# Kernel optimization log

Hardware: AMD Instinct MI355X
Metric: run time of the kernel (lower is better)

## Reference

```python
import jax, jax.numpy as jnp
import numpy as np

EMBED_DIM = 256
NUM_HEADS = 4
LN_EPS = 1e-5


def setup_inputs() -> dict:
    b, n, e = 2, 4096, EMBED_DIM
    key = jax.random.key(0)
    ks = jax.random.split(key, 12)
    x = jax.random.normal(ks[0], (b, n, e), dtype=jnp.float32)
    # rotary cache: cos/sin of random angles, shape [2, b, n, e, 1]
    ang = jax.random.uniform(ks[1], (b, n, e, 1), dtype=jnp.float32) * (2 * np.pi)
    encoding = jnp.stack([jnp.cos(ang), jnp.sin(ang)], axis=0)
    s_e = 1.0 / np.sqrt(e)
    s_2e = 1.0 / np.sqrt(2 * e)
    Wqkv_w = jax.random.normal(ks[2], (3 * e, e), dtype=jnp.float32) * s_e
    Wqkv_b = jax.random.normal(ks[3], (3 * e,), dtype=jnp.float32) * s_e
    out_w = jax.random.normal(ks[4], (e, e), dtype=jnp.float32) * s_e
    out_b = jax.random.normal(ks[5], (e,), dtype=jnp.float32) * s_e
    ffn1_w = jax.random.normal(ks[6], (2 * e, 2 * e), dtype=jnp.float32) * s_2e
    ffn1_b = jax.random.normal(ks[7], (2 * e,), dtype=jnp.float32) * s_2e
    ln_g = jnp.ones((2 * e,), dtype=jnp.float32)
    ln_b = jnp.zeros((2 * e,), dtype=jnp.float32)
    ffn2_w = jax.random.normal(ks[8], (e, 2 * e), dtype=jnp.float32) * s_2e
    ffn2_b = jax.random.normal(ks[9], (e,), dtype=jnp.float32) * s_2e
    return {"x": x, "encoding": encoding, "Wqkv_w": Wqkv_w, "Wqkv_b": Wqkv_b,
            "out_w": out_w, "out_b": out_b, "ffn1_w": ffn1_w, "ffn1_b": ffn1_b,
            "ln_g": ln_g, "ln_b": ln_b, "ffn2_w": ffn2_w, "ffn2_b": ffn2_b}


def _forward(x, encoding, Wqkv_w, Wqkv_b, out_w, out_b, ffn1_w, ffn1_b, ln_g, ln_b, ffn2_w, ffn2_b):
    b, n, e = x.shape
    h = NUM_HEADS
    hd = e // h
    qkv = x @ Wqkv_w.T + Wqkv_b                      # [b,n,3e]
    qkv = qkv.reshape(b, n, e, 3)
    qk, v = qkv[..., :2], qkv[..., 2]                # [b,n,e,2], [b,n,e]
    # rotate_half: interpret e as (h, hd//2, 2) pairs, rotate within pairs
    r = qk.reshape(b, n, h, hd // 2, 2, 2)
    r = jnp.stack([-r[..., 1, :], r[..., 0, :]], axis=4).reshape(b, n, e, 2)
    qk = qk * encoding[0] + r * encoding[1]          # cached rotary emb
    q = qk[..., 0].reshape(b, n, h, hd)
    k = qk[..., 1].reshape(b, n, h, hd)
    vh = v.reshape(b, n, h, hd)
    scale = 1.0 / np.sqrt(hd).astype(np.float32)
    scores = jnp.einsum('bqhd,bkhd->bhqk', q, k) * scale
    attn = jax.nn.softmax(scores, axis=-1)
    ctx = jnp.einsum('bhqk,bkhd->bqhd', attn, vh).reshape(b, n, e)
    message = ctx @ out_w.T + out_b
    y = jnp.concatenate([x, message], axis=2)        # [b,n,2e]
    y = y @ ffn1_w.T + ffn1_b
    mu = jnp.mean(y, axis=-1, keepdims=True)
    var = jnp.mean(jnp.square(y - mu), axis=-1, keepdims=True)
    y = (y - mu) * jax.lax.rsqrt(var + LN_EPS) * ln_g + ln_b
    y = jax.nn.gelu(y, approximate=False)            # torch nn.GELU default = exact
    y = y @ ffn2_w.T + ffn2_b
    return x + y


def reference(x, encoding, Wqkv_w, Wqkv_b, out_w, out_b, ffn1_w, ffn1_b, ln_g, ln_b, ffn2_w, ffn2_b):
    return _forward(x, encoding, Wqkv_w, Wqkv_b, out_w, out_b, ffn1_w, ffn1_b, ln_g, ln_b, ffn2_w, ffn2_b)
```

## Files before the change

### kernel.cpp

```cpp
#include <hip/hip_runtime.h>
#include <hip/hip_bf16.h>

using u16 = unsigned short;
using u16x8 = __attribute__((ext_vector_type(8))) unsigned short;
using s16x4 = __attribute__((ext_vector_type(4))) short;
using s16x8 = __attribute__((ext_vector_type(8))) short;
using f32x4 = __attribute__((ext_vector_type(4))) float;

__device__ __forceinline__ f32x4 mfma16(s16x8 a, s16x8 b, f32x4 c) {
    return __builtin_amdgcn_mfma_f32_16x16x32_bf16(a, b, c, 0, 0, 0);
}

__device__ __forceinline__ u16 f2bf(float f) {
    union { float f; unsigned u; } v; v.f = f;
    unsigned r = v.u + 0x7FFFu + ((v.u >> 16) & 1u);
    return (u16)(r >> 16);
}

__device__ __forceinline__ unsigned cvt_pk_bf16(float lo, float hi) {
    unsigned r;
    asm("v_cvt_pk_bf16_f32 %0, %1, %2" : "=v"(r) : "v"(lo), "v"(hi));
    return r;
}

__device__ __forceinline__ float fast_exp2(float x) {
    float r;
    asm("v_exp_f32 %0, %1" : "=v"(r) : "v"(x));
    return r;
}

__device__ __forceinline__ unsigned pk2(u16 a, u16 b) {
    return (unsigned)a | ((unsigned)b << 16);
}

__device__ __forceinline__ float bf2f(u16 u) {
    union { unsigned u; float f; } v; v.u = ((unsigned)u) << 16;
    return v.f;
}

__device__ __forceinline__ void gload_lds16(const u16* g, u16* l) {
    __builtin_amdgcn_global_load_lds(
        (const __attribute__((address_space(1))) void*)g,
        (__attribute__((address_space(3))) void*)l, 16, 0, 0);
}

__global__ __launch_bounds__(256) void conv_kernel(
    const float* __restrict__ s0, const float* __restrict__ s1,
    const float* __restrict__ s2, const float* __restrict__ s3,
    const float* __restrict__ s4,
    u16* __restrict__ d0, u16* __restrict__ d1, u16* __restrict__ d2,
    u16* __restrict__ d3, u16* __restrict__ d4)
{
    int i = blockIdx.x * 256 + threadIdx.x;
    const float* s; u16* d; int off;
    if (i < 524288)      { s = s0; d = d0; off = i; }
    else if (i < 573440) { s = s1; d = d1; off = i - 524288; }
    else if (i < 589824) { s = s2; d = d2; off = i - 573440; }
    else if (i < 655360) { s = s3; d = d3; off = i - 589824; }
    else                 { s = s4; d = d4; off = i - 655360; }
    float4 f = ((const float4*)s)[off];
    ushort4 u;
    u.x = f2bf(f.x); u.y = f2bf(f.y); u.z = f2bf(f.z); u.w = f2bf(f.w);
    ((ushort4*)d)[off] = u;
}

template<int OUTMODE, bool SPLIT, bool RESID>
__global__ __launch_bounds__(256) void gemm_kernel(
    const u16* __restrict__ A0, const u16* __restrict__ A1,
    const u16* __restrict__ W, const float* __restrict__ bias,
    const float* __restrict__ resid, float* __restrict__ outf,
    u16* __restrict__ outb, int M, int N, int K)
{
    __shared__ u16 A_lds[3][128][64];
    __shared__ u16 B_lds[3][64][64];
    const int tid = threadIdx.x;
    const int l = tid & 63, w = tid >> 6;
    const int lr = l & 15, lg = l >> 4;
    const int r7 = lr & 7;
    const int m0 = blockIdx.x * 128, n0 = blockIdx.y * 64;
    const int wm = (w >> 1) * 64, wn = (w & 1) * 32;

    const int lrow = l >> 3;
    const int swz = (l & 7) ^ lrow;
    const int arow = 32 * w + lrow;
    const int brow = 16 * w + lrow;

    #define STAGE_G(s, b)                                                     \
        do {                                                                  \
            int k0_ = 64 * (s);                                               \
            const u16* As_; int lda_;                                         \
            if (SPLIT) {                                                      \
                lda_ = 256;                                                   \
                As_ = (k0_ < 256) ? (A0 + k0_) : (A1 + (k0_ - 256));          \
            } else { lda_ = K; As_ = A0 + k0_; }                              \
            _Pragma("unroll")                                                 \
            for (int i = 0; i < 4; ++i)                                       \
                gload_lds16(As_ + (size_t)(m0 + arow + 8 * i) * lda_ + swz * 8,\
                            &A_lds[b][32 * w + 8 * i][0]);                    \
            _Pragma("unroll")                                                 \
            for (int i = 0; i < 2; ++i)                                       \
                gload_lds16(W + (size_t)(n0 + brow + 8 * i) * K + k0_ + swz * 8,\
                            &B_lds[b][16 * w + 8 * i][0]);                    \
        } while (0)

    f32x4 acc[4][2];
    #pragma unroll
    for (int i = 0; i < 4; ++i)
        #pragma unroll
        for (int j = 0; j < 2; ++j)
            acc[i][j] = (f32x4){0.f, 0.f, 0.f, 0.f};

    const int NS = K >> 6;
    int cur = 0, nxt = 1;
    STAGE_G(0, 0);

    for (int s = 0; s < NS; ++s) {
        if (s + 1 < NS) {
            STAGE_G(s + 1, nxt);
            asm volatile("s_waitcnt vmcnt(6)" ::: "memory");
        } else {
            asm volatile("s_waitcnt vmcnt(0)" ::: "memory");
        }
        __builtin_amdgcn_sched_barrier(0);
        __builtin_amdgcn_s_barrier();
        __builtin_amdgcn_sched_barrier(0);

        #pragma unroll
        for (int ks = 0; ks < 2; ++ks) {
            s16x8 af[4], bfr[2];
            #pragma unroll
            for (int ms = 0; ms < 4; ++ms)
                af[ms] = *(const s16x8*)&A_lds[cur][wm + ms * 16 + lr]
                                              [((ks * 4 + lg) ^ r7) * 8];
            #pragma unroll
            for (int ns = 0; ns < 2; ++ns)
                bfr[ns] = *(const s16x8*)&B_lds[cur][wn + ns * 16 + lr]
                                               [((ks * 4 + lg) ^ r7) * 8];
            #pragma unroll
            for (int ms = 0; ms < 4; ++ms)
                #pragma unroll
                for (int ns = 0; ns < 2; ++ns)
                    acc[ms][ns] = mfma16(af[ms], bfr[ns], acc[ms][ns]);
        }
        cur = nxt;
        nxt = (nxt == 2) ? 0 : nxt + 1;
    }
    #undef STAGE_G

    #pragma unroll
    for (int ms = 0; ms < 4; ++ms) {
        #pragma unroll
        for (int ns = 0; ns < 2; ++ns) {
            int cg = n0 + wn + ns * 16 + lr;
            float bv = bias[cg];
            #pragma unroll
            for (int r = 0; r < 4; ++r) {
                int rg = m0 + wm + ms * 16 + lg * 4 + r;
                float val = acc[ms][ns][r] + bv;
                if (RESID) val += resid[(size_t)rg * N + cg];
                if (OUTMODE == 0) outf[(size_t)rg * N + cg] = val;
                else              outb[(size_t)rg * N + cg] = f2bf(val);
            }
        }
    }
}

__global__ __launch_bounds__(256) void rope_kernel(
    const u16* __restrict__ qkv, const float* __restrict__ enc,
    u16* __restrict__ Qo, u16* __restrict__ Ko, u16* __restrict__ Vo)
{
    int idx = blockIdx.x * 256 + threadIdx.x;
    int row = idx >> 7;
    int p = idx & 127;
    int c0 = p * 2;
    const u16* base = qkv + (size_t)row * 768 + p * 6;
    ushort2 a01 = *(const ushort2*)(base);
    ushort2 a23 = *(const ushort2*)(base + 2);
    ushort2 a45 = *(const ushort2*)(base + 4);
    float q0 = bf2f(a01.x), k0 = bf2f(a01.y);
    float q1 = bf2f(a23.y), k1 = bf2f(a45.x);
    const float* cb = enc + (size_t)row * 256 + c0;
    float2 cosv = *(const float2*)cb;
    float2 sinv = *(const float2*)(cb + 2097152);
    float qr0 = q0 * cosv.x - q1 * sinv.x;
    float qr1 = q1 * cosv.y + q0 * sinv.y;
    float kr0 = k0 * cosv.x - k1 * sinv.x;
    float kr1 = k1 * cosv.y + k0 * sinv.y;
    const float qs = 0.18033688011112042f;
    qr0 *= qs; qr1 *= qs;
    int h = c0 >> 6, d = c0 & 63;
    int b = row >> 12, n = row & 4095;
    size_t o = (((size_t)(b * 4 + h)) * 4096 + n) * 64 + d;
    *(unsigned*)(Qo + o) = cvt_pk_bf16(qr0, qr1);
    *(unsigned*)(Ko + o) = cvt_pk_bf16(kr0, kr1);
    *(unsigned*)(Vo + o) = pk2(a23.x, a45.y);
}

__global__ __launch_bounds__(256) void transpose_v(
    const u16* __restrict__ V, u16* __restrict__ Vt)
{
    __shared__ u16 t[64][72];
    int bh = blockIdx.y, n0 = blockIdx.x * 64;
    int tid = threadIdx.x;
    #pragma unroll
    for (int i = 0; i < 2; ++i) {
        int c = tid + 256 * i;
        int r = c >> 3, cg = c & 7;
        *(uint4*)&t[r][cg * 8] =
            *(const uint4*)(V + ((size_t)bh * 4096 + n0 + r) * 64 + cg * 8);
    }
    __syncthreads();
    #pragma unroll
    for (int i = 0; i < 2; ++i) {
        int c = tid + 256 * i;
        int d = c >> 3, ng = c & 7;
        unsigned w0 = pk2(t[ng*8+0][d], t[ng*8+1][d]);
        unsigned w1 = pk2(t[ng*8+2][d], t[ng*8+3][d]);
        unsigned w2 = pk2(t[ng*8+4][d], t[ng*8+5][d]);
        unsigned w3 = pk2(t[ng*8+6][d], t[ng*8+7][d]);
        uint4 o4 = make_uint4(w0, w1, w2, w3);
        *(uint4*)(Vt + ((size_t)bh * 64 + d) * 4096 + n0 + ng * 8) = o4;
    }
}

__global__ __launch_bounds__(256) void attn_kernel(
    const u16* __restrict__ Qp, const u16* __restrict__ Kp,
    const u16* __restrict__ Vtp, u16* __restrict__ Opart,
    float* __restrict__ Ssum)
{
    __shared__ u16 K_lds[3][64][64];
    __shared__ u16 V_lds[3][64][64];
    const int tid = threadIdx.x;
    const int l = tid & 63, w = tid >> 6;
    const int lr = l & 15, lg = l >> 4;
    const int bh = blockIdx.y, z = blockIdx.z;
    const int n0 = blockIdx.x * 64 + w * 16;

    const u16* Qb = Qp + ((size_t)bh * 4096 + n0) * 64;
    s16x8 qf0 = *(const s16x8*)(Qb + lr * 64 + lg * 8);
    s16x8 qf1 = *(const s16x8*)(Qb + lr * 64 + 32 + lg * 8);

    const u16* Kb = Kp + (size_t)bh * 4096 * 64 + (size_t)z * 1024 * 64;
    const u16* Vb = Vtp + (size_t)bh * 64 * 4096 + z * 1024;

    const int swz = (l & 7) ^ ((l >> 3) & 7);
    const int row0 = 16 * w + (l >> 3);
    const size_t koff0 = (size_t)row0 * 64 + swz * 8;
    const size_t koff1 = (size_t)(row0 + 8) * 64 + swz * 8;
    const size_t voff0 = (size_t)row0 * 4096 + swz * 8;
    const size_t voff1 = (size_t)(row0 + 8) * 4096 + swz * 8;

    #define STAGE(kt, b)                                                      \
        do {                                                                  \
            const u16* ks_ = Kb + (size_t)(kt) * 4096;                        \
            const u16* vs_ = Vb + (size_t)(kt) * 64;                          \
            gload_lds16(ks_ + koff0, &K_lds[b][16 * w][0]);                   \
            gload_lds16(ks_ + koff1, &K_lds[b][16 * w + 8][0]);               \
            gload_lds16(vs_ + voff0, &V_lds[b][16 * w][0]);                   \
            gload_lds16(vs_ + voff1, &V_lds[b][16 * w + 8][0]);               \
        } while (0)

    f32x4 O[4];
    #pragma unroll
    for (int dv = 0; dv < 4; ++dv) O[dv] = (f32x4){0.f, 0.f, 0.f, 0.f};
    f32x4 ssum = (f32x4){0.f, 0.f, 0.f, 0.f};
    s16x8 ones;
    #pragma unroll
    for (int j = 0; j < 8; ++j) ones[j] = (short)0x3F80;

    const int r7 = lr & 7;
    int cur = 0, nxt = 1;
    STAGE(0, 0);

    for (int kt = 0; kt < 16; ++kt) {
        if (kt + 1 < 16) {
            STAGE(kt + 1, nxt);
            asm volatile("s_waitcnt vmcnt(4)" ::: "memory");
        } else {
            asm volatile("s_waitcnt vmcnt(0)" ::: "memory");
        }
        __builtin_amdgcn_sched_barrier(0);
        __builtin_amdgcn_s_barrier();
        __builtin_amdgcn_sched_barrier(0);

        f32x4 S[4];
        #pragma unroll
        for (int v4 = 0; v4 < 4; ++v4) {
            const int krow = v4 * 16 + lr;
            s16x8 kf0 = *(const s16x8*)&K_lds[cur][krow][(lg ^ r7) * 8];
            s16x8 kf1 = *(const s16x8*)&K_lds[cur][krow][((4 + lg) ^ r7) * 8];
            f32x4 zz = (f32x4){-24.f, -24.f, -24.f, -24.f};
            zz = mfma16(kf0, qf0, zz);
            zz = mfma16(kf1, qf1, zz);
            S[v4] = zz;
        }

        float p[4][4];
        #pragma unroll
        for (int v4 = 0; v4 < 4; ++v4)
            #pragma unroll
            for (int r = 0; r < 4; ++r)
                p[v4][r] = fast_exp2(S[v4][r]);

        s16x8 pa[2];
        #pragma unroll
        for (int kb = 0; kb < 2; ++kb) {
            union { unsigned u[4]; s16x8 v; } pu;
            pu.u[0] = cvt_pk_bf16(p[2*kb][0],   p[2*kb][1]);
            pu.u[1] = cvt_pk_bf16(p[2*kb][2],   p[2*kb][3]);
            pu.u[2] = cvt_pk_bf16(p[2*kb+1][0], p[2*kb+1][1]);
            pu.u[3] = cvt_pk_bf16(p[2*kb+1][2], p[2*kb+1][3]);
            pa[kb] = pu.v;
        }

        #pragma unroll
        for (int dv = 0; dv < 4; ++dv) {
            const int vrow = 16 * dv + lr;
            #pragma unroll
            for (int kb = 0; kb < 2; ++kb) {
                const int c16a = 4 * kb + (lg >> 1);
                const u16* vpa = &V_lds[cur][vrow][((c16a      ^ r7) * 8) + 4 * (lg & 1)];
                const u16* vpb = &V_lds[cur][vrow][(((c16a + 2) ^ r7) * 8) + 4 * (lg & 1)];
                s16x4 va  = *(const s16x4*)vpa;
                s16x4 vb4 = *(const s16x4*)vpb;
                s16x8 vf = __builtin_shufflevector(va, vb4, 0,1,2,3,4,5,6,7);
                O[dv] = mfma16(pa[kb], vf, O[dv]);
            }
        }
        ssum = mfma16(pa[0], ones, ssum);
        ssum = mfma16(pa[1], ones, ssum);

        cur = nxt;
        nxt = (nxt == 2) ? 0 : nxt + 1;
    }
    #undef STAGE

    u16* Ob = Opart + ((size_t)(z * 8 + bh) * 4096 + n0) * 64;
    #pragma unroll
    for (int dv = 0; dv < 4; ++dv)
        #pragma unroll
        for (int r = 0; r < 4; ++r)
            Ob[(size_t)(4 * lg + r) * 64 + 16 * dv + lr] = f2bf(O[dv][r]);
    if (lr == 0) {
        float4 sv = make_float4(ssum[0], ssum[1], ssum[2], ssum[3]);
        *(float4*)&Ssum[(size_t)(z * 8 + bh) * 4096 + n0 + 4 * lg] = sv;
    }
}

__global__ __launch_bounds__(256) void combine_kernel(
    const u16* __restrict__ Opart, const float* __restrict__ Ssum,
    u16* __restrict__ ctx)
{
    int idx = blockIdx.x * 256 + threadIdx.x;
    int rr = idx >> 3;
    int dc = (idx & 7) * 8;
    float s = Ssum[rr] + Ssum[32768 + rr] + Ssum[65536 + rr] + Ssum[98304 + rr];
    float inv = 1.f / s;
    float acc[8];
    #pragma unroll
    for (int j = 0; j < 8; ++j) acc[j] = 0.f;
    #pragma unroll
    for (int z = 0; z < 4; ++z) {
        u16x8 ov = *(const u16x8*)(Opart + ((size_t)z * 32768 + rr) * 64 + dc);
        #pragma unroll
        for (int j = 0; j < 8; ++j) acc[j] += bf2f(ov[j]);
    }
    #pragma unroll
    for (int j = 0; j < 8; ++j) acc[j] *= inv;
    int bh = rr >> 12, n = rr & 4095;
    int b = bh >> 2, h = bh & 3;
    uint4 o4 = make_uint4(cvt_pk_bf16(acc[0], acc[1]), cvt_pk_bf16(acc[2], acc[3]),
                          cvt_pk_bf16(acc[4], acc[5]), cvt_pk_bf16(acc[6], acc[7]));
    *(uint4*)(ctx + ((size_t)(b * 4096 + n)) * 256 + h * 64 + dc) = o4;
}

__global__ __launch_bounds__(256) void ln_gelu_kernel(
    const float* __restrict__ y, const float* __restrict__ g,
    const float* __restrict__ bta, u16* __restrict__ o)
{
    int row = blockIdx.x * 4 + (threadIdx.x >> 6);
    int l = threadIdx.x & 63;
    const float* yr = y + (size_t)row * 512 + l * 8;
    float4 va = *(const float4*)yr;
    float4 vb = *(const float4*)(yr + 4);
    float v[8] = {va.x, va.y, va.z, va.w, vb.x, vb.y, vb.z, vb.w};
    float s = 0.f;
    #pragma unroll
    for (int j = 0; j < 8; ++j) s += v[j];
    #pragma unroll
    for (int off = 32; off; off >>= 1) s += __shfl_xor(s, off, 64);
    float mu = s * (1.f / 512.f);
    float q = 0.f;
    #pragma unroll
    for (int j = 0; j < 8; ++j) { float t = v[j] - mu; q += t * t; }
    #pragma unroll
    for (int off = 32; off; off >>= 1) q += __shfl_xor(q, off, 64);
    float rs = rsqrtf(q * (1.f / 512.f) + 1e-5f);
    u16 u[8];
    #pragma unroll
    for (int j = 0; j < 8; ++j) {
        float t = (v[j] - mu) * rs * g[l * 8 + j] + bta[l * 8 + j];
        t = t * 0.5f * (1.f + erff(t * 0.70710678118654752f));
        u[j] = f2bf(t);
    }
    uint4 o4 = make_uint4(pk2(u[0], u[1]), pk2(u[2], u[3]),
                          pk2(u[4], u[5]), pk2(u[6], u[7]));
    *(uint4*)(o + (size_t)row * 512 + l * 8) = o4;
}

extern "C" void kernel_launch(void* const* d_in, const int* in_sizes, int n_in,
                              void* d_out, int out_size, void* d_ws, size_t ws_size,
                              hipStream_t stream) {
    (void)in_sizes; (void)n_in; (void)out_size; (void)ws_size;
    const float* x    = (const float*)d_in[0];
    const float* enc  = (const float*)d_in[1];
    const float* wqkv = (const float*)d_in[2];
    const float* bqkv = (const float*)d_in[3];
    const float* wout = (const float*)d_in[4];
    const float* bout = (const float*)d_in[5];
    const float* w1   = (const float*)d_in[6];
    const float* b1   = (const float*)d_in[7];
    const float* lng  = (const float*)d_in[8];
    const float* lnb  = (const float*)d_in[9];
    const float* w2   = (const float*)d_in[10];
    const float* b2   = (const float*)d_in[11];
    float* out = (float*)d_out;
    char* ws = (char*)d_ws;

    u16*   xb    = (u16*)(ws + 0);
    u16*   wqkvb = (u16*)(ws + 4194304);
    u16*   woutb = (u16*)(ws + 4587520);
    u16*   w1b   = (u16*)(ws + 4718592);
    u16*   w2b   = (u16*)(ws + 5242880);
    u16*   qkvb  = (u16*)(ws + 5505024);
    u16*   OpartB= (u16*)(ws + 5505024);
    float* y1    = (float*)(ws + 5505024);
    float* Ssum  = (float*)(ws + 22282240);
    u16*   q     = (u16*)(ws + 30670848);
    u16*   k     = (u16*)(ws + 34865152);
    u16*   v     = (u16*)(ws + 39059456);
    u16*   vt    = (u16*)(ws + 43253760);
    u16*   ybf   = q;
    u16*   ctx   = (u16*)(ws + 47448064);
    u16*   msg   = (u16*)(ws + 51642368);

    conv_kernel<<<2688, 256, 0, stream>>>(x, wqkv, wout, w1, w2,
                                          xb, wqkvb, woutb, w1b, w2b);
    gemm_kernel<1, false, false><<<dim3(64, 12), 256, 0, stream>>>(
        xb, nullptr, wqkvb, bqkv, nullptr, nullptr, qkvb, 8192, 768, 256);
    rope_kernel<<<4096, 256, 0, stream>>>(qkvb, enc, q, k, v);
    transpose_v<<<dim3(64, 8), 256, 0, stream>>>(v, vt);
    attn_kernel<<<dim3(64, 8, 4), 256, 0, stream>>>(q, k, vt, OpartB, Ssum);
    combine_kernel<<<1024, 256, 0, stream>>>(OpartB, Ssum, ctx);
    gemm_kernel<1, false, false><<<dim3(64, 4), 256, 0, stream>>>(
        ctx, nullptr, woutb, bout, nullptr, nullptr, msg, 8192, 256, 256);
    gemm_kernel<0, true, false><<<dim3(64, 8), 256, 0, stream>>>(
        xb, msg, w1b, b1, nullptr, y1, nullptr, 8192, 512, 512);
    ln_gelu_kernel<<<2048, 256, 0, stream>>>(y1, lng, lnb, ybf);
    gemm_kernel<0, false, true><<<dim3(64, 4), 256, 0, stream>>>(
        ybf, nullptr, w2b, b2, x, out, nullptr, 8192, 256, 512);
}
```

Baseline: 135.3 us.

## Process two query tiles per wave in attention and permute V transpose layout

Each wave now handles 32 query rows (two 16-row tiles) so every K/V fragment loaded from LDS feeds twice as many MFMAs, and the grid is halved. The V transpose stores columns in an interleaved order so the PV step can read one 8-element vector instead of two 4-element pieces. The triple-buffered pipeline with manual vmcnt waits becomes double buffering with __syncthreads, which cuts LDS use but may expose more load latency. Register pressure rises from the doubled accumulators, and the grid drops to 1024 blocks.

```diff
diff --git a/kernel.cpp b/kernel.cpp
--- a/kernel.cpp
+++ b/kernel.cpp
@@ -214,10 +214,12 @@
     for (int i = 0; i < 2; ++i) {
         int c = tid + 256 * i;
         int d = c >> 3, ng = c & 7;
-        unsigned w0 = pk2(t[ng*8+0][d], t[ng*8+1][d]);
-        unsigned w1 = pk2(t[ng*8+2][d], t[ng*8+3][d]);
-        unsigned w2 = pk2(t[ng*8+4][d], t[ng*8+5][d]);
-        unsigned w3 = pk2(t[ng*8+6][d], t[ng*8+7][d]);
+        int kb = ng >> 2, lg4 = ng & 3;
+        int base = 32 * kb + 4 * lg4;
+        unsigned w0 = pk2(t[base +  0][d], t[base +  1][d]);
+        unsigned w1 = pk2(t[base +  2][d], t[base +  3][d]);
+        unsigned w2 = pk2(t[base + 16][d], t[base + 17][d]);
+        unsigned w3 = pk2(t[base + 18][d], t[base + 19][d]);
         uint4 o4 = make_uint4(w0, w1, w2, w3);
         *(uint4*)(Vt + ((size_t)bh * 64 + d) * 4096 + n0 + ng * 8) = o4;
     }
@@ -228,17 +230,22 @@
     const u16* __restrict__ Vtp, u16* __restrict__ Opart,
     float* __restrict__ Ssum)
 {
-    __shared__ u16 K_lds[3][64][64];
-    __shared__ u16 V_lds[3][64][64];
+    __shared__ u16 K_lds[2][64][64];
+    __shared__ u16 V_lds[2][64][64];
     const int tid = threadIdx.x;
     const int l = tid & 63, w = tid >> 6;
     const int lr = l & 15, lg = l >> 4;
+    const int r7 = lr & 7;
     const int bh = blockIdx.y, z = blockIdx.z;
-    const int n0 = blockIdx.x * 64 + w * 16;
+    const int n0 = blockIdx.x * 128 + w * 32;
 
     const u16* Qb = Qp + ((size_t)bh * 4096 + n0) * 64;
-    s16x8 qf0 = *(const s16x8*)(Qb + lr * 64 + lg * 8);
-    s16x8 qf1 = *(const s16x8*)(Qb + lr * 64 + 32 + lg * 8);
+    s16x8 qf[2][2];
+    #pragma unroll
+    for (int qt = 0; qt < 2; ++qt)
+        #pragma unroll
+        for (int dh = 0; dh < 2; ++dh)
+            qf[qt][dh] = *(const s16x8*)(Qb + (qt * 16 + lr) * 64 + dh * 32 + lg * 8);
 
     const u16* Kb = Kp + (size_t)bh * 4096 * 64 + (size_t)z * 1024 * 64;
     const u16* Vb = Vtp + (size_t)bh * 64 * 4096 + z * 1024;
@@ -260,57 +267,59 @@
             gload_lds16(vs_ + voff1, &V_lds[b][16 * w + 8][0]);               \
         } while (0)
 
-    f32x4 O[4];
-    #pragma unroll
-    for (int dv = 0; dv < 4; ++dv) O[dv] = (f32x4){0.f, 0.f, 0.f, 0.f};
-    f32x4 ssum = (f32x4){0.f, 0.f, 0.f, 0.f};
+    f32x4 O[2][4];
+    #pragma unroll
+    for (int qt = 0; qt < 2; ++qt)
+        #pragma unroll
+        for (int dv = 0; dv < 4; ++dv)
+            O[qt][dv] = (f32x4){0.f, 0.f, 0.f, 0.f};
+    f32x4 ssum[2];
+    ssum[0] = (f32x4){0.f, 0.f, 0.f, 0.f};
+    ssum[1] = (f32x4){0.f, 0.f, 0.f, 0.f};
     s16x8 ones;
     #pragma unroll
     for (int j = 0; j < 8; ++j) ones[j] = (short)0x3F80;
 
-    const int r7 = lr & 7;
-    int cur = 0, nxt = 1;
     STAGE(0, 0);
+    __syncthreads();
 
     for (int kt = 0; kt < 16; ++kt) {
-        if (kt + 1 < 16) {
-            STAGE(kt + 1, nxt);
-            asm volatile("s_waitcnt vmcnt(4)" ::: "memory");
-        } else {
-            asm volatile("s_waitcnt vmcnt(0)" ::: "memory");
-        }
-        __builtin_amdgcn_sched_barrier(0);
-        __builtin_amdgcn_s_barrier();
-        __builtin_amdgcn_sched_barrier(0);
-
-        f32x4 S[4];
+        const int cur = kt & 1;
+        if (kt + 1 < 16) STAGE(kt + 1, cur ^ 1);
+
+        f32x4 S[2][4];
         #pragma unroll
         for (int v4 = 0; v4 < 4; ++v4) {
             const int krow = v4 * 16 + lr;
             s16x8 kf0 = *(const s16x8*)&K_lds[cur][krow][(lg ^ r7) * 8];
             s16x8 kf1 = *(const s16x8*)&K_lds[cur][krow][((4 + lg) ^ r7) * 8];
-            f32x4 zz = (f32x4){-24.f, -24.f, -24.f, -24.f};
-            zz = mfma16(kf0, qf0, zz);
-            zz = mfma16(kf1, qf1, zz);
-            S[v4] = zz;
-        }
-
-        float p[4][4];
-        #pragma unroll
-        for (int v4 = 0; v4 < 4; ++v4)
-            #pragma unroll
-            for (int r = 0; r < 4; ++r)
-                p[v4][r] = fast_exp2(S[v4][r]);
-
-        s16x8 pa[2];
-        #pragma unroll
-        for (int kb = 0; kb < 2; ++kb) {
-            union { unsigned u[4]; s16x8 v; } pu;
-            pu.u[0] = cvt_pk_bf16(p[2*kb][0],   p[2*kb][1]);
-            pu.u[1] = cvt_pk_bf16(p[2*kb][2],   p[2*kb][3]);
-            pu.u[2] = cvt_pk_bf16(p[2*kb+1][0], p[2*kb+1][1]);
-            pu.u[3] = cvt_pk_bf16(p[2*kb+1][2], p[2*kb+1][3]);
-            pa[kb] = pu.v;
+            #pragma unroll
+            for (int qt = 0; qt < 2; ++qt) {
+                f32x4 zz = (f32x4){-24.f, -24.f, -24.f, -24.f};
+                zz = mfma16(kf0, qf[qt][0], zz);
+                zz = mfma16(kf1, qf[qt][1], zz);
+                S[qt][v4] = zz;
+            }
+        }
+
+        s16x8 pa[2][2];
+        #pragma unroll
+        for (int qt = 0; qt < 2; ++qt) {
+            float p[4][4];
+            #pragma unroll
+            for (int v4 = 0; v4 < 4; ++v4)
+                #pragma unroll
+                for (int r = 0; r < 4; ++r)
+                    p[v4][r] = fast_exp2(S[qt][v4][r]);
+            #pragma unroll
+            for (int kb = 0; kb < 2; ++kb) {
+                union { unsigned u[4]; s16x8 v; } pu;
+                pu.u[0] = cvt_pk_bf16(p[2*kb][0],   p[2*kb][1]);
+                pu.u[1] = cvt_pk_bf16(p[2*kb][2],   p[2*kb][3]);
+                pu.u[2] = cvt_pk_bf16(p[2*kb+1][0], p[2*kb+1][1]);
+                pu.u[3] = cvt_pk_bf16(p[2*kb+1][2], p[2*kb+1][3]);
+                pa[qt][kb] = pu.v;
+            }
         }
 
         #pragma unroll
@@ -318,32 +327,38 @@
             const int vrow = 16 * dv + lr;
             #pragma unroll
             for (int kb = 0; kb < 2; ++kb) {
-                const int c16a = 4 * kb + (lg >> 1);
-                const u16* vpa = &V_lds[cur][vrow][((c16a      ^ r7) * 8) + 4 * (lg & 1)];
-                const u16* vpb = &V_lds[cur][vrow][(((c16a + 2) ^ r7) * 8) + 4 * (lg & 1)];
-                s16x4 va  = *(const s16x4*)vpa;
-                s16x4 vb4 = *(const s16x4*)vpb;
-                s16x8 vf = __builtin_shufflevector(va, vb4, 0,1,2,3,4,5,6,7);
-                O[dv] = mfma16(pa[kb], vf, O[dv]);
+                s16x8 vf = *(const s16x8*)&V_lds[cur][vrow][((4 * kb + lg) ^ r7) * 8];
+                #pragma unroll
+                for (int qt = 0; qt < 2; ++qt)
+                    O[qt][dv] = mfma16(pa[qt][kb], vf, O[qt][dv]);
             }
         }
-        ssum = mfma16(pa[0], ones, ssum);
-        ssum = mfma16(pa[1], ones, ssum);
-
-        cur = nxt;
-        nxt = (nxt == 2) ? 0 : nxt + 1;
+        #pragma unroll
+        for (int qt = 0; qt < 2; ++qt) {
+            ssum[qt] = mfma16(pa[qt][0], ones, ssum[qt]);
+            ssum[qt] = mfma16(pa[qt][1], ones, ssum[qt]);
+        }
+
+        __syncthreads();
     }
     #undef STAGE
 
     u16* Ob = Opart + ((size_t)(z * 8 + bh) * 4096 + n0) * 64;
     #pragma unroll
-    for (int dv = 0; dv < 4; ++dv)
-        #pragma unroll
-        for (int r = 0; r < 4; ++r)
-            Ob[(size_t)(4 * lg + r) * 64 + 16 * dv + lr] = f2bf(O[dv][r]);
+    for (int qt = 0; qt < 2; ++qt)
+        #pragma unroll
+        for (int dv = 0; dv < 4; ++dv)
+            #pragma unroll
+            for (int r = 0; r < 4; ++r)
+                Ob[(size_t)(qt * 16 + 4 * lg + r) * 64 + 16 * dv + lr] =
+                    f2bf(O[qt][dv][r]);
     if (lr == 0) {
-        float4 sv = make_float4(ssum[0], ssum[1], ssum[2], ssum[3]);
-        *(float4*)&Ssum[(size_t)(z * 8 + bh) * 4096 + n0 + 4 * lg] = sv;
+        #pragma unroll
+        for (int qt = 0; qt < 2; ++qt) {
+            float4 sv = make_float4(ssum[qt][0], ssum[qt][1],
+                                    ssum[qt][2], ssum[qt][3]);
+            *(float4*)&Ssum[(size_t)(z * 8 + bh) * 4096 + n0 + qt * 16 + 4 * lg] = sv;
+        }
     }
 }
 
@@ -450,7 +465,7 @@
         xb, nullptr, wqkvb, bqkv, nullptr, nullptr, qkvb, 8192, 768, 256);
     rope_kernel<<<4096, 256, 0, stream>>>(qkvb, enc, q, k, v);
     transpose_v<<<dim3(64, 8), 256, 0, stream>>>(v, vt);
-    attn_kernel<<<dim3(64, 8, 4), 256, 0, stream>>>(q, k, vt, OpartB, Ssum);
+    attn_kernel<<<dim3(32, 8, 4), 256, 0, stream>>>(q, k, vt, OpartB, Ssum);
     combine_kernel<<<1024, 256, 0, stream>>>(OpartB, Ssum, ctx);
     gemm_kernel<1, false, false><<<dim3(64, 4), 256, 0, stream>>>(
         ctx, nullptr, woutb, bout, nullptr, nullptr, msg, 8192, 256, 256);
```

Measured after the change: 129.4 us. 1.05x faster.
